# Kernel tuning notes

Hardware: AMD Instinct MI355X
Metric: run time of the kernel (lower is better)

## Reference

```python
import jax, jax.numpy as jnp
import numpy as np

B, N, C = 16, 64, 512


def _ln(x, g, b, eps=1e-5):
    m = x.mean(-1, keepdims=True)
    v = ((x - m) ** 2).mean(-1, keepdims=True)
    return (x - m) * jax.lax.rsqrt(v + eps) * g + b


def _layer(x, edge, WA, WB, WE, WU, WV, ge, be, gv, bv):
    # x: (B, N, C); edge: (B, N, N, C) with edge[b, i, j] for pair (end=i, start=j)
    n = x.shape[1]
    res = x
    Vix = x @ WA.T  # end-node (i) features
    Vjx = x @ WB.T  # start-node (j) features
    e_lin = edge @ WE.T
    # 'ev,bvc->bec' with end/start one-hots == broadcast gather over i / j
    m = Vix[:, :, None, :] + Vjx[:, None, :, :] + e_lin
    edge = edge + jax.nn.relu(_ln(m, ge, be))
    e = jax.nn.softmax(jax.nn.sigmoid(edge), axis=2)  # softmax over start-node axis j
    Ujx = x @ WV.T  # gathered at start node j
    # end.T scatter == sum over j of e[b,i,j,c] * Ujx[b,j,c]
    agg = jnp.einsum('bijc,bjc->bic', e, Ujx) / n
    x = x @ WU.T + agg
    x = jax.nn.relu(res + _ln(x, gv, bv))
    return x, edge


def setup_inputs() -> dict:
    key = jax.random.key(0)
    ks = jax.random.split(key, 12)
    scale = float(np.sqrt(2.0 / C))
    inp = {
        "x": jax.random.normal(ks[0], (B, N, C), jnp.float32),
        "edge": jax.random.normal(ks[1], (B, N * N, C), jnp.float32),
    }
    names = ["WA1", "WB1", "WE1", "WU1", "WV1", "WA2", "WB2", "WE2", "WU2", "WV2"]
    for i, nm in enumerate(names):
        inp[nm] = jax.random.normal(ks[2 + i], (C, C), jnp.float32) * scale
    for nm in ["ge1", "gv1", "ge2", "gv2"]:
        inp[nm] = jnp.ones((C,), jnp.float32)
    for nm in ["be1", "bv1", "be2", "bv2"]:
        inp[nm] = jnp.zeros((C,), jnp.float32)
    return inp


def reference(x, edge, WA1, WB1, WE1, WU1, WV1, WA2, WB2, WE2, WU2, WV2,
              ge1, be1, gv1, bv1, ge2, be2, gv2, bv2):
    b, _, c = edge.shape
    n = x.shape[1]
    edge = edge.reshape(b, n, n, c)
    x, edge = _layer(x, edge, WA1, WB1, WE1, WU1, WV1, ge1, be1, gv1, bv1)
    x, edge = _layer(x, edge, WA2, WB2, WE2, WU2, WV2, ge2, be2, gv2, bv2)
    return x, edge.reshape(b, n * n, c)
```

## Files before the change

kernel.cpp:

```cpp
#include <hip/hip_runtime.h>
#include <math.h>

#define CD 512
#define NNODE 64
#define TPAD 520

typedef __attribute__((ext_vector_type(8)))  short bfrag8;
typedef __attribute__((ext_vector_type(4)))  short sv4;
typedef __attribute__((ext_vector_type(4)))  float f32x4;
typedef __attribute__((ext_vector_type(16))) float f32x16;

__device__ __forceinline__ unsigned short f2bf(float f) {
    union { float f; unsigned u; } v; v.f = f;
    unsigned r = (v.u + 0x7fffu + ((v.u >> 16) & 1u)) >> 16;
    return (unsigned short)r;
}
__device__ __forceinline__ float bf2f(unsigned short u) {
    union { unsigned u; float f; } v; v.u = ((unsigned)u) << 16;
    return v.f;
}

__global__ void pack16_k(const float* __restrict__ W0, const float* __restrict__ W1,
                         const float* __restrict__ W2, const float* __restrict__ W3,
                         const float* __restrict__ W4, const float* __restrict__ W5,
                         const float* __restrict__ W6, const float* __restrict__ W7,
                         unsigned short* __restrict__ out)
{
    const float* Ws[8] = {W0,W1,W2,W3,W4,W5,W6,W7};
    int kt = blockIdx.x, ct = blockIdx.y, wi = blockIdx.z, l = threadIdx.x;
    const float* W = Ws[wi];
    int c  = ct * 16 + (l & 15);
    int k0 = kt * 32 + (l >> 4) * 8;
    const float* src = W + (size_t)c * CD + k0;
    unsigned short o[8];
    #pragma unroll
    for (int i = 0; i < 8; ++i) o[i] = f2bf(src[i]);
    unsigned short* dst = out + (size_t)wi * 262144 + ((size_t)(kt * 32 + ct) * 64 + l) * 8;
    *(bfrag8*)dst = *(bfrag8*)o;
}

__global__ void pack32_k(const float* __restrict__ W0, const float* __restrict__ W1,
                         unsigned short* __restrict__ out)
{
    const float* Ws[2] = {W0,W1};
    int kt = blockIdx.x, ct = blockIdx.y, wi = blockIdx.z, l = threadIdx.x;
    const float* W = Ws[wi];
    int c  = ct * 32 + (l & 31);
    int k0 = kt * 16 + (l >> 5) * 8;
    const float* src = W + (size_t)c * CD + k0;
    unsigned short o[8];
    #pragma unroll
    for (int i = 0; i < 8; ++i) o[i] = f2bf(src[i]);
    unsigned short* dst = out + (size_t)wi * 262144 + ((size_t)(kt * 16 + ct) * 64 + l) * 8;
    *(bfrag8*)dst = *(bfrag8*)o;
}

__global__ __launch_bounds__(256, 2) void gemm4_mfma(
    const float* __restrict__ A, const unsigned short* __restrict__ Bp4,
    float* __restrict__ O0, float* __restrict__ O1,
    float* __restrict__ O2, float* __restrict__ O3)
{
    __shared__ unsigned short atile[16 * TPAD];
    const int rb = blockIdx.x * 16, widx = blockIdx.y;
    float* outs[4] = {O0,O1,O2,O3};
    float* out = outs[widx];
    const unsigned short* Bp = Bp4 + (size_t)widx * 262144;
    const int t = threadIdx.x, l = t & 63, v = t >> 6;

    #pragma unroll
    for (int it = 0; it < 8; ++it) {
        int flat = it * 1024 + t * 4;
        float4 x4 = *(const float4*)(A + (size_t)rb * CD + flat);
        int r = flat >> 9, c = flat & 511;
        sv4 pk; pk.x = (short)f2bf(x4.x); pk.y = (short)f2bf(x4.y);
        pk.z = (short)f2bf(x4.z); pk.w = (short)f2bf(x4.w);
        *(sv4*)(atile + r * TPAD + c) = pk;
    }
    __syncthreads();

    f32x4 acc[8] = {};
    const unsigned short* aptr = atile + (size_t)(l & 15) * TPAD + (l >> 4) * 8;
    const unsigned short* bptr = Bp + (size_t)(v * 8) * 512 + (size_t)l * 8;

    bfrag8 a0, a1, b0[8], b1[8];
    a0 = *(const bfrag8*)aptr;
    #pragma unroll
    for (int tt = 0; tt < 8; ++tt) b0[tt] = *(const bfrag8*)(bptr + tt * 512);
    for (int k2 = 0; k2 < 8; ++k2) {
        int kt1 = 2 * k2 + 1;
        a1 = *(const bfrag8*)(aptr + kt1 * 32);
        #pragma unroll
        for (int tt = 0; tt < 8; ++tt) b1[tt] = *(const bfrag8*)(bptr + (size_t)kt1 * 16384 + tt * 512);
        #pragma unroll
        for (int tt = 0; tt < 8; ++tt)
            acc[tt] = __builtin_amdgcn_mfma_f32_16x16x32_bf16(a0, b0[tt], acc[tt], 0, 0, 0);
        int kt2 = (k2 == 7) ? 15 : (2 * k2 + 2);
        a0 = *(const bfrag8*)(aptr + kt2 * 32);
        #pragma unroll
        for (int tt = 0; tt < 8; ++tt) b0[tt] = *(const bfrag8*)(bptr + (size_t)kt2 * 16384 + tt * 512);
        #pragma unroll
        for (int tt = 0; tt < 8; ++tt)
            acc[tt] = __builtin_amdgcn_mfma_f32_16x16x32_bf16(a1, b1[tt], acc[tt], 0, 0, 0);
    }
    #pragma unroll
    for (int tt = 0; tt < 8; ++tt) {
        int c = (v * 8 + tt) * 16 + (l & 15);
        #pragma unroll
        for (int r = 0; r < 4; ++r) {
            int row = rb + (l >> 4) * 4 + r;
            out[(size_t)row * CD + c] = acc[tt][r];
        }
    }
}

__global__ __launch_bounds__(512, 2) void edge_mfma(
    const float* __restrict__ ein, float* __restrict__ eout,
    const float* __restrict__ Vix, const float* __restrict__ Vjx,
    const float* __restrict__ Ujx, const unsigned short* __restrict__ Bp,
    const float* __restrict__ ge, const float* __restrict__ be,
    float* __restrict__ agg)
{
    __shared__ unsigned short tile[2 * 64 * TPAD];
    __shared__ float sums[128][2][2];

    const int q = blockIdx.x;
    const int b = q >> 5, i0 = q & 31;
    const int bi0 = b * 64 + i0;
    const int t = threadIdx.x, l = t & 63, w = t >> 6;
    const int stripe = w & 3, H = w >> 2, p = stripe >> 1;
    const int brow = b * 64;

    #pragma unroll
    for (int p2 = 0; p2 < 2; ++p2) {
        const float* src = ein + (size_t)(bi0 + p2 * 32) * 32768;
        unsigned short* dst = tile + p2 * 64 * TPAD;
        #pragma unroll 4
        for (int it = 0; it < 16; ++it) {
            int flat = it * 2048 + t * 4;
            float4 v4 = *(const float4*)(src + flat);
            int r = flat >> 9, c = flat & 511;
            sv4 pk; pk.x = (short)f2bf(v4.x); pk.y = (short)f2bf(v4.y);
            pk.z = (short)f2bf(v4.z); pk.w = (short)f2bf(v4.w);
            *(sv4*)(dst + r * TPAD + c) = pk;
        }
    }
    __syncthreads();

    f32x16 acc[8] = {};
    const unsigned short* aptr = tile + (size_t)(stripe * 32 + (l & 31)) * TPAD + (l >> 5) * 8;
    const unsigned short* bptr = Bp + (size_t)(H * 8) * 512 + (size_t)l * 8;

    bfrag8 a0, a1, b0[8], b1[8];
    a0 = *(const bfrag8*)aptr;
    #pragma unroll
    for (int tt = 0; tt < 8; ++tt) b0[tt] = *(const bfrag8*)(bptr + tt * 512);
    for (int k2 = 0; k2 < 16; ++k2) {
        int kt1 = 2 * k2 + 1;
        a1 = *(const bfrag8*)(aptr + kt1 * 16);
        #pragma unroll
        for (int tt = 0; tt < 8; ++tt) b1[tt] = *(const bfrag8*)(bptr + (size_t)kt1 * 8192 + tt * 512);
        #pragma unroll
        for (int tt = 0; tt < 8; ++tt)
            acc[tt] = __builtin_amdgcn_mfma_f32_32x32x16_bf16(a0, b0[tt], acc[tt], 0, 0, 0);
        int kt2 = (k2 == 15) ? 31 : (2 * k2 + 2);
        a0 = *(const bfrag8*)(aptr + kt2 * 16);
        #pragma unroll
        for (int tt = 0; tt < 8; ++tt) b0[tt] = *(const bfrag8*)(bptr + (size_t)kt2 * 8192 + tt * 512);
        #pragma unroll
        for (int tt = 0; tt < 8; ++tt)
            acc[tt] = __builtin_amdgcn_mfma_f32_32x32x16_bf16(a1, b1[tt], acc[tt], 0, 0, 0);
    }

    const int cbase = H * 256 + (l & 31);
    const int biP = bi0 + p * 32;
    float vix[8], gev[8], bev[8];
    #pragma unroll
    for (int tt = 0; tt < 8; ++tt) {
        int c = cbase + tt * 32;
        vix[tt] = Vix[(size_t)biP * CD + c];
        gev[tt] = ge[c]; bev[tt] = be[c];
    }
    float s1[16], s2[16];
    #pragma unroll
    for (int r = 0; r < 16; ++r) {
        int rl = (r & 3) + 8 * (r >> 2) + 4 * (l >> 5);
        int rt = stripe * 32 + rl;
        int j = rt & 63;
        const float* vjr = Vjx + (size_t)(brow + j) * CD;
        float a1_ = 0.f, a2_ = 0.f;
        #pragma unroll
        for (int tt = 0; tt < 8; ++tt) {
            float m = acc[tt][r] + vix[tt] + vjr[cbase + tt * 32];
            acc[tt][r] = m;
            a1_ += m; a2_ = fmaf(m, m, a2_);
        }
        s1[r] = a1_; s2[r] = a2_;
    }
    #pragma unroll
    for (int off = 1; off < 32; off <<= 1) {
        #pragma unroll
        for (int r = 0; r < 16; ++r) {
            s1[r] += __shfl_xor(s1[r], off, 64);
            s2[r] += __shfl_xor(s2[r], off, 64);
        }
    }
    if ((l & 31) == 0) {
        #pragma unroll
        for (int r = 0; r < 16; ++r) {
            int rl = (r & 3) + 8 * (r >> 2) + 4 * (l >> 5);
            int rt = stripe * 32 + rl;
            sums[rt][H][0] = s1[r]; sums[rt][H][1] = s2[r];
        }
    }
    __syncthreads();

    #pragma unroll
    for (int r = 0; r < 16; ++r) {
        int rl = (r & 3) + 8 * (r >> 2) + 4 * (l >> 5);
        int rt = stripe * 32 + rl;
        float t1 = sums[rt][0][0] + sums[rt][1][0];
        float t2 = sums[rt][0][1] + sums[rt][1][1];
        float mean = t1 * (1.f / 512.f);
        float var  = t2 * (1.f / 512.f) - mean * mean;
        float rs   = rsqrtf(var + 1e-5f);
        int j = rt & 63;
        unsigned short* trow = tile + (size_t)rt * TPAD;
        float* erow = eout + ((size_t)biP * 64 + j) * CD;
        #pragma unroll
        for (int tt = 0; tt < 8; ++tt) {
            int c = cbase + tt * 32;
            float ln  = (acc[tt][r] - mean) * rs * gev[tt] + bev[tt];
            float env = bf2f(trow[c]) + fmaxf(ln, 0.f);
            erow[c] = env;
            float sg = 1.f / (1.f + __expf(-env));
            trow[c] = f2bf(__expf(sg));
        }
    }
    __syncthreads();

    {
        int c = t;
        #pragma unroll
        for (int pp = 0; pp < 2; ++pp) {
            const unsigned short* tp = tile + pp * 64 * TPAD;
            const float* uj = Ujx + (size_t)brow * CD + c;
            float den = 0.f, num = 0.f;
            #pragma unroll 8
            for (int j = 0; j < NNODE; ++j) {
                float wv = bf2f(tp[j * TPAD + c]);
                float uv = uj[(size_t)j * CD];
                den += wv; num = fmaf(wv, uv, num);
            }
            agg[(size_t)(bi0 + pp * 32) * CD + c] = num / (den * (float)NNODE);
        }
    }
}

__global__ __launch_bounds__(256) void xupd_kernel(
    const float* __restrict__ res,
    const float* __restrict__ XU,
    const float* __restrict__ aggp,
    const float* __restrict__ gv, const float* __restrict__ bv,
    float* __restrict__ xout)
{
    int r = blockIdx.x * 4 + (threadIdx.x >> 6);
    int lane = threadIdx.x & 63;
    const float* xu = XU + (size_t)r * CD;
    const float* ag = aggp + (size_t)r * CD;
    float y[8]; float s1 = 0.f, s2 = 0.f;
    #pragma unroll
    for (int u = 0; u < 8; ++u) {
        int c = lane + u * 64;
        float v = xu[c] + ag[c];
        y[u] = v; s1 += v; s2 += v * v;
    }
    #pragma unroll
    for (int off = 32; off > 0; off >>= 1) {
        s1 += __shfl_xor(s1, off, 64);
        s2 += __shfl_xor(s2, off, 64);
    }
    float mean = s1 * (1.f / 512.f);
    float var  = s2 * (1.f / 512.f) - mean * mean;
    float rs   = rsqrtf(var + 1e-5f);
    const float* rr = res + (size_t)r * CD;
    float* xo = xout + (size_t)r * CD;
    #pragma unroll
    for (int u = 0; u < 8; ++u) {
        int c = lane + u * 64;
        float ln = (y[u] - mean) * rs * gv[c] + bv[c];
        xo[c] = fmaxf(rr[c] + ln, 0.f);
    }
}

extern "C" void kernel_launch(void* const* d_in, const int* in_sizes, int n_in,
                              void* d_out, int out_size, void* d_ws, size_t ws_size,
                              hipStream_t stream)
{
    const float* x    = (const float*)d_in[0];
    const float* edge = (const float*)d_in[1];
    const float* W[10];
    for (int i = 0; i < 10; ++i) W[i] = (const float*)d_in[2 + i];
    const float* ge1 = (const float*)d_in[12];
    const float* gv1 = (const float*)d_in[13];
    const float* ge2 = (const float*)d_in[14];
    const float* gv2 = (const float*)d_in[15];
    const float* be1 = (const float*)d_in[16];
    const float* bv1 = (const float*)d_in[17];
    const float* be2 = (const float*)d_in[18];
    const float* bv2 = (const float*)d_in[19];

    char* wsb = (char*)d_ws;
    unsigned short* P16 = (unsigned short*)wsb;
    unsigned short* P32 = (unsigned short*)(wsb + (size_t)4  * 1048576);
    float* Vix = (float*)(wsb + (size_t)5  * 1048576);
    float* Vjx = (float*)(wsb + (size_t)7  * 1048576);
    float* Ujx = (float*)(wsb + (size_t)9  * 1048576);
    float* XU  = (float*)(wsb + (size_t)11 * 1048576);
    float* agg = (float*)(wsb + (size_t)13 * 1048576);
    float* x1  = (float*)(wsb + (size_t)15 * 1048576);

    float* xout = (float*)d_out;
    float* eint = xout + (size_t)524288;

    pack16_k<<<dim3(16, 32, 8), 64, 0, stream>>>(
        W[0], W[1], W[4], W[3], W[5], W[6], W[9], W[8], P16);
    pack32_k<<<dim3(32, 16, 2), 64, 0, stream>>>(W[2], W[7], P32);

    gemm4_mfma<<<dim3(64, 4), 256, 0, stream>>>(x, P16, Vix, Vjx, Ujx, XU);
    edge_mfma<<<512, 512, 0, stream>>>(edge, eint, Vix, Vjx, Ujx, P32, ge1, be1, agg);
    xupd_kernel<<<256, 256, 0, stream>>>(x, XU, agg, gv1, bv1, x1);
    gemm4_mfma<<<dim3(64, 4), 256, 0, stream>>>(x1, P16 + (size_t)4 * 262144, Vix, Vjx, Ujx, XU);
    edge_mfma<<<512, 512, 0, stream>>>(eint, eint, Vix, Vjx, Ujx, P32 + 262144, ge2, be2, agg);
    xupd_kernel<<<256, 256, 0, stream>>>(x1, XU, agg, gv2, bv2, xout);
}
```

Before: 591.7 us.

## Store intermediate edge tensor in bf16 and retile edge/projection kernels per node row

The layer-1 edge output is now written as bf16 into the output buffer and read back as bf16 by layer 2, which is meant to cut memory traffic on the largest tensor. The edge kernel now handles one end-node row per block (1024 blocks, occupancy hint raised to 4) with fewer accumulators per wave, and the node projection GEMM switches to 32x32 MFMA tiles over 64-row blocks. All weight packing goes through a single pack kernel. The trade-off is extra rounding in the residual edge carried between layers, which costs some accuracy.

```diff
diff --git a/kernel.cpp b/kernel.cpp
--- a/kernel.cpp
+++ b/kernel.cpp
@@ -6,8 +6,8 @@
 #define TPAD 520
 
 typedef __attribute__((ext_vector_type(8)))  short bfrag8;
+typedef __attribute__((ext_vector_type(8)))  short sv8;
 typedef __attribute__((ext_vector_type(4)))  short sv4;
-typedef __attribute__((ext_vector_type(4)))  float f32x4;
 typedef __attribute__((ext_vector_type(16))) float f32x16;
 
 __device__ __forceinline__ unsigned short f2bf(float f) {
@@ -20,29 +20,14 @@
     return v.f;
 }
 
-__global__ void pack16_k(const float* __restrict__ W0, const float* __restrict__ W1,
+__global__ void pack32_k(const float* __restrict__ W0, const float* __restrict__ W1,
                          const float* __restrict__ W2, const float* __restrict__ W3,
                          const float* __restrict__ W4, const float* __restrict__ W5,
                          const float* __restrict__ W6, const float* __restrict__ W7,
+                         const float* __restrict__ W8, const float* __restrict__ W9,
                          unsigned short* __restrict__ out)
 {
-    const float* Ws[8] = {W0,W1,W2,W3,W4,W5,W6,W7};
-    int kt = blockIdx.x, ct = blockIdx.y, wi = blockIdx.z, l = threadIdx.x;
-    const float* W = Ws[wi];
-    int c  = ct * 16 + (l & 15);
-    int k0 = kt * 32 + (l >> 4) * 8;
-    const float* src = W + (size_t)c * CD + k0;
-    unsigned short o[8];
-    #pragma unroll
-    for (int i = 0; i < 8; ++i) o[i] = f2bf(src[i]);
-    unsigned short* dst = out + (size_t)wi * 262144 + ((size_t)(kt * 32 + ct) * 64 + l) * 8;
-    *(bfrag8*)dst = *(bfrag8*)o;
-}
-
-__global__ void pack32_k(const float* __restrict__ W0, const float* __restrict__ W1,
-                         unsigned short* __restrict__ out)
-{
-    const float* Ws[2] = {W0,W1};
+    const float* Ws[10] = {W0,W1,W2,W3,W4,W5,W6,W7,W8,W9};
     int kt = blockIdx.x, ct = blockIdx.y, wi = blockIdx.z, l = threadIdx.x;
     const float* W = Ws[wi];
     int c  = ct * 32 + (l & 31);
@@ -55,85 +40,92 @@
     *(bfrag8*)dst = *(bfrag8*)o;
 }
 
-__global__ __launch_bounds__(256, 2) void gemm4_mfma(
+__global__ __launch_bounds__(512, 4) void proj_mfma(
     const float* __restrict__ A, const unsigned short* __restrict__ Bp4,
     float* __restrict__ O0, float* __restrict__ O1,
     float* __restrict__ O2, float* __restrict__ O3)
 {
-    __shared__ unsigned short atile[16 * TPAD];
-    const int rb = blockIdx.x * 16, widx = blockIdx.y;
+    __shared__ unsigned short tile[64 * TPAD];
+    const int rb = blockIdx.x * 64, widx = blockIdx.y;
     float* outs[4] = {O0,O1,O2,O3};
     float* out = outs[widx];
     const unsigned short* Bp = Bp4 + (size_t)widx * 262144;
-    const int t = threadIdx.x, l = t & 63, v = t >> 6;
-
-    #pragma unroll
-    for (int it = 0; it < 8; ++it) {
-        int flat = it * 1024 + t * 4;
-        float4 x4 = *(const float4*)(A + (size_t)rb * CD + flat);
+    const int t = threadIdx.x, l = t & 63, w = t >> 6;
+    const int stripe = w & 1, H = w >> 1;
+
+    const float* src = A + (size_t)rb * CD;
+    #pragma unroll 4
+    for (int it = 0; it < 16; ++it) {
+        int flat = it * 2048 + t * 4;
+        float4 v4 = *(const float4*)(src + flat);
         int r = flat >> 9, c = flat & 511;
-        sv4 pk; pk.x = (short)f2bf(x4.x); pk.y = (short)f2bf(x4.y);
-        pk.z = (short)f2bf(x4.z); pk.w = (short)f2bf(x4.w);
-        *(sv4*)(atile + r * TPAD + c) = pk;
+        sv4 pk; pk.x = (short)f2bf(v4.x); pk.y = (short)f2bf(v4.y);
+        pk.z = (short)f2bf(v4.z); pk.w = (short)f2bf(v4.w);
+        *(sv4*)(tile + r * TPAD + c) = pk;
     }
     __syncthreads();
 
-    f32x4 acc[8] = {};
-    const unsigned short* aptr = atile + (size_t)(l & 15) * TPAD + (l >> 4) * 8;
-    const unsigned short* bptr = Bp + (size_t)(v * 8) * 512 + (size_t)l * 8;
-
-    bfrag8 a0, a1, b0[8], b1[8];
+    f32x16 acc[4] = {};
+    const unsigned short* aptr = tile + (size_t)(stripe * 32 + (l & 31)) * TPAD + (l >> 5) * 8;
+    const unsigned short* bptr = Bp + ((size_t)(H * 4) * 64 + l) * 8;
+
+    bfrag8 a0, a1, b0[4], b1[4];
     a0 = *(const bfrag8*)aptr;
     #pragma unroll
-    for (int tt = 0; tt < 8; ++tt) b0[tt] = *(const bfrag8*)(bptr + tt * 512);
-    for (int k2 = 0; k2 < 8; ++k2) {
+    for (int tt = 0; tt < 4; ++tt) b0[tt] = *(const bfrag8*)(bptr + tt * 512);
+    for (int k2 = 0; k2 < 16; ++k2) {
         int kt1 = 2 * k2 + 1;
-        a1 = *(const bfrag8*)(aptr + kt1 * 32);
-        #pragma unroll
-        for (int tt = 0; tt < 8; ++tt) b1[tt] = *(const bfrag8*)(bptr + (size_t)kt1 * 16384 + tt * 512);
-        #pragma unroll
-        for (int tt = 0; tt < 8; ++tt)
-            acc[tt] = __builtin_amdgcn_mfma_f32_16x16x32_bf16(a0, b0[tt], acc[tt], 0, 0, 0);
-        int kt2 = (k2 == 7) ? 15 : (2 * k2 + 2);
-        a0 = *(const bfrag8*)(aptr + kt2 * 32);
-        #pragma unroll
-        for (int tt = 0; tt < 8; ++tt) b0[tt] = *(const bfrag8*)(bptr + (size_t)kt2 * 16384 + tt * 512);
-        #pragma unroll
-        for (int tt = 0; tt < 8; ++tt)
-            acc[tt] = __builtin_amdgcn_mfma_f32_16x16x32_bf16(a1, b1[tt], acc[tt], 0, 0, 0);
-    }
-    #pragma unroll
-    for (int tt = 0; tt < 8; ++tt) {
-        int c = (v * 8 + tt) * 16 + (l & 15);
-        #pragma unroll
-        for (int r = 0; r < 4; ++r) {
-            int row = rb + (l >> 4) * 4 + r;
-            out[(size_t)row * CD + c] = acc[tt][r];
-        }
-    }
-}
-
-__global__ __launch_bounds__(512, 2) void edge_mfma(
-    const float* __restrict__ ein, float* __restrict__ eout,
+        a1 = *(const bfrag8*)(aptr + kt1 * 16);
+        #pragma unroll
+        for (int tt = 0; tt < 4; ++tt) b1[tt] = *(const bfrag8*)(bptr + (size_t)kt1 * 8192 + tt * 512);
+        #pragma unroll
+        for (int tt = 0; tt < 4; ++tt)
+            acc[tt] = __builtin_amdgcn_mfma_f32_32x32x16_bf16(a0, b0[tt], acc[tt], 0, 0, 0);
+        int kt2 = (k2 == 15) ? 31 : (2 * k2 + 2);
+        a0 = *(const bfrag8*)(aptr + kt2 * 16);
+        #pragma unroll
+        for (int tt = 0; tt < 4; ++tt) b0[tt] = *(const bfrag8*)(bptr + (size_t)kt2 * 8192 + tt * 512);
+        #pragma unroll
+        for (int tt = 0; tt < 4; ++tt)
+            acc[tt] = __builtin_amdgcn_mfma_f32_32x32x16_bf16(a1, b1[tt], acc[tt], 0, 0, 0);
+    }
+    const int cbase = H * 128 + (l & 31);
+    #pragma unroll
+    for (int r = 0; r < 16; ++r) {
+        int rl = (r & 3) + 8 * (r >> 2) + 4 * (l >> 5);
+        int row = rb + stripe * 32 + rl;
+        #pragma unroll
+        for (int tt = 0; tt < 4; ++tt)
+            out[(size_t)row * CD + cbase + tt * 32] = acc[tt][r];
+    }
+}
+
+template<bool INBF, bool OUTBF>
+__global__ __launch_bounds__(512, 4) void edge_mfma(
+    const void* __restrict__ einv, void* __restrict__ eoutv,
     const float* __restrict__ Vix, const float* __restrict__ Vjx,
     const float* __restrict__ Ujx, const unsigned short* __restrict__ Bp,
     const float* __restrict__ ge, const float* __restrict__ be,
     float* __restrict__ agg)
 {
-    __shared__ unsigned short tile[2 * 64 * TPAD];
-    __shared__ float sums[128][2][2];
-
-    const int q = blockIdx.x;
-    const int b = q >> 5, i0 = q & 31;
-    const int bi0 = b * 64 + i0;
+    __shared__ unsigned short tile[64 * TPAD];
+    __shared__ float sums[64][4][2];
+
+    const int bi = blockIdx.x;
+    const int brow = bi & ~63;
     const int t = threadIdx.x, l = t & 63, w = t >> 6;
-    const int stripe = w & 3, H = w >> 2, p = stripe >> 1;
-    const int brow = b * 64;
-
-    #pragma unroll
-    for (int p2 = 0; p2 < 2; ++p2) {
-        const float* src = ein + (size_t)(bi0 + p2 * 32) * 32768;
-        unsigned short* dst = tile + p2 * 64 * TPAD;
+    const int stripe = w & 1, H = w >> 1;
+
+    if (INBF) {
+        const unsigned short* src = (const unsigned short*)einv + (size_t)bi * 65536;
+        #pragma unroll 4
+        for (int it = 0; it < 8; ++it) {
+            int flat = it * 4096 + t * 8;
+            int r = flat >> 9, c = flat & 511;
+            *(sv8*)(tile + r * TPAD + c) = *(const sv8*)(src + flat);
+        }
+    } else {
+        const float* src = (const float*)einv + (size_t)bi * 32768;
         #pragma unroll 4
         for (int it = 0; it < 16; ++it) {
             int flat = it * 2048 + t * 4;
@@ -141,43 +133,42 @@
             int r = flat >> 9, c = flat & 511;
             sv4 pk; pk.x = (short)f2bf(v4.x); pk.y = (short)f2bf(v4.y);
             pk.z = (short)f2bf(v4.z); pk.w = (short)f2bf(v4.w);
-            *(sv4*)(dst + r * TPAD + c) = pk;
+            *(sv4*)(tile + r * TPAD + c) = pk;
         }
     }
     __syncthreads();
 
-    f32x16 acc[8] = {};
+    f32x16 acc[4] = {};
     const unsigned short* aptr = tile + (size_t)(stripe * 32 + (l & 31)) * TPAD + (l >> 5) * 8;
-    const unsigned short* bptr = Bp + (size_t)(H * 8) * 512 + (size_t)l * 8;
-
-    bfrag8 a0, a1, b0[8], b1[8];
+    const unsigned short* bptr = Bp + ((size_t)(H * 4) * 64 + l) * 8;
+
+    bfrag8 a0, a1, b0[4], b1[4];
     a0 = *(const bfrag8*)aptr;
     #pragma unroll
-    for (int tt = 0; tt < 8; ++tt) b0[tt] = *(const bfrag8*)(bptr + tt * 512);
+    for (int tt = 0; tt < 4; ++tt) b0[tt] = *(const bfrag8*)(bptr + tt * 512);
     for (int k2 = 0; k2 < 16; ++k2) {
         int kt1 = 2 * k2 + 1;
         a1 = *(const bfrag8*)(aptr + kt1 * 16);
         #pragma unroll
-        for (int tt = 0; tt < 8; ++tt) b1[tt] = *(const bfrag8*)(bptr + (size_t)kt1 * 8192 + tt * 512);
-        #pragma unroll
-        for (int tt = 0; tt < 8; ++tt)
+        for (int tt = 0; tt < 4; ++tt) b1[tt] = *(const bfrag8*)(bptr + (size_t)kt1 * 8192 + tt * 512);
+        #pragma unroll
+        for (int tt = 0; tt < 4; ++tt)
             acc[tt] = __builtin_amdgcn_mfma_f32_32x32x16_bf16(a0, b0[tt], acc[tt], 0, 0, 0);
         int kt2 = (k2 == 15) ? 31 : (2 * k2 + 2);
         a0 = *(const bfrag8*)(aptr + kt2 * 16);
         #pragma unroll
-        for (int tt = 0; tt < 8; ++tt) b0[tt] = *(const bfrag8*)(bptr + (size_t)kt2 * 8192 + tt * 512);
-        #pragma unroll
-        for (int tt = 0; tt < 8; ++tt)
+        for (int tt = 0; tt < 4; ++tt) b0[tt] = *(const bfrag8*)(bptr + (size_t)kt2 * 8192 + tt * 512);
+        #pragma unroll
+        for (int tt = 0; tt < 4; ++tt)
             acc[tt] = __builtin_amdgcn_mfma_f32_32x32x16_bf16(a1, b1[tt], acc[tt], 0, 0, 0);
     }
 
-    const int cbase = H * 256 + (l & 31);
-    const int biP = bi0 + p * 32;
-    float vix[8], gev[8], bev[8];
-    #pragma unroll
-    for (int tt = 0; tt < 8; ++tt) {
+    const int cbase = H * 128 + (l & 31);
+    float vix[4], gev[4], bev[4];
+    #pragma unroll
+    for (int tt = 0; tt < 4; ++tt) {
         int c = cbase + tt * 32;
-        vix[tt] = Vix[(size_t)biP * CD + c];
+        vix[tt] = Vix[(size_t)bi * CD + c];
         gev[tt] = ge[c]; bev[tt] = be[c];
     }
     float s1[16], s2[16];
@@ -185,11 +176,10 @@
     for (int r = 0; r < 16; ++r) {
         int rl = (r & 3) + 8 * (r >> 2) + 4 * (l >> 5);
         int rt = stripe * 32 + rl;
-        int j = rt & 63;
-        const float* vjr = Vjx + (size_t)(brow + j) * CD;
+        const float* vjr = Vjx + (size_t)(brow + rt) * CD;
         float a1_ = 0.f, a2_ = 0.f;
         #pragma unroll
-        for (int tt = 0; tt < 8; ++tt) {
+        for (int tt = 0; tt < 4; ++tt) {
             float m = acc[tt][r] + vix[tt] + vjr[cbase + tt * 32];
             acc[tt][r] = m;
             a1_ += m; a2_ = fmaf(m, m, a2_);
@@ -218,20 +208,19 @@
     for (int r = 0; r < 16; ++r) {
         int rl = (r & 3) + 8 * (r >> 2) + 4 * (l >> 5);
         int rt = stripe * 32 + rl;
-        float t1 = sums[rt][0][0] + sums[rt][1][0];
-        float t2 = sums[rt][0][1] + sums[rt][1][1];
+        float t1 = sums[rt][0][0] + sums[rt][1][0] + sums[rt][2][0] + sums[rt][3][0];
+        float t2 = sums[rt][0][1] + sums[rt][1][1] + sums[rt][2][1] + sums[rt][3][1];
         float mean = t1 * (1.f / 512.f);
         float var  = t2 * (1.f / 512.f) - mean * mean;
         float rs   = rsqrtf(var + 1e-5f);
-        int j = rt & 63;
         unsigned short* trow = tile + (size_t)rt * TPAD;
-        float* erow = eout + ((size_t)biP * 64 + j) * CD;
-        #pragma unroll
-        for (int tt = 0; tt < 8; ++tt) {
+        #pragma unroll
+        for (int tt = 0; tt < 4; ++tt) {
             int c = cbase + tt * 32;
             float ln  = (acc[tt][r] - mean) * rs * gev[tt] + bev[tt];
             float env = bf2f(trow[c]) + fmaxf(ln, 0.f);
-            erow[c] = env;
+            if (OUTBF) ((unsigned short*)eoutv)[(size_t)bi * 65536 + rt * 512 + c] = f2bf(env);
+            else       ((float*)eoutv)[(size_t)bi * 32768 + rt * 512 + c] = env;
             float sg = 1.f / (1.f + __expf(-env));
             trow[c] = f2bf(__expf(sg));
         }
@@ -240,19 +229,15 @@
 
     {
         int c = t;
-        #pragma unroll
-        for (int pp = 0; pp < 2; ++pp) {
-            const unsigned short* tp = tile + pp * 64 * TPAD;
-            const float* uj = Ujx + (size_t)brow * CD + c;
-            float den = 0.f, num = 0.f;
-            #pragma unroll 8
-            for (int j = 0; j < NNODE; ++j) {
-                float wv = bf2f(tp[j * TPAD + c]);
-                float uv = uj[(size_t)j * CD];
-                den += wv; num = fmaf(wv, uv, num);
-            }
-            agg[(size_t)(bi0 + pp * 32) * CD + c] = num / (den * (float)NNODE);
-        }
+        const float* uj = Ujx + (size_t)brow * CD + c;
+        float den = 0.f, num = 0.f;
+        #pragma unroll 8
+        for (int j = 0; j < NNODE; ++j) {
+            float wv = bf2f(tile[j * TPAD + c]);
+            float uv = uj[(size_t)j * CD];
+            den += wv; num = fmaf(wv, uv, num);
+        }
+        agg[(size_t)bi * CD + c] = num / (den * (float)NNODE);
     }
 }
 
@@ -310,26 +295,28 @@
     const float* bv2 = (const float*)d_in[19];
 
     char* wsb = (char*)d_ws;
-    unsigned short* P16 = (unsigned short*)wsb;
-    unsigned short* P32 = (unsigned short*)(wsb + (size_t)4  * 1048576);
-    float* Vix = (float*)(wsb + (size_t)5  * 1048576);
-    float* Vjx = (float*)(wsb + (size_t)7  * 1048576);
-    float* Ujx = (float*)(wsb + (size_t)9  * 1048576);
-    float* XU  = (float*)(wsb + (size_t)11 * 1048576);
-    float* agg = (float*)(wsb + (size_t)13 * 1048576);
-    float* x1  = (float*)(wsb + (size_t)15 * 1048576);
-
-    float* xout = (float*)d_out;
-    float* eint = xout + (size_t)524288;
-
-    pack16_k<<<dim3(16, 32, 8), 64, 0, stream>>>(
-        W[0], W[1], W[4], W[3], W[5], W[6], W[9], W[8], P16);
-    pack32_k<<<dim3(32, 16, 2), 64, 0, stream>>>(W[2], W[7], P32);
-
-    gemm4_mfma<<<dim3(64, 4), 256, 0, stream>>>(x, P16, Vix, Vjx, Ujx, XU);
-    edge_mfma<<<512, 512, 0, stream>>>(edge, eint, Vix, Vjx, Ujx, P32, ge1, be1, agg);
+    unsigned short* P32 = (unsigned short*)wsb;
+    float* Vix = (float*)(wsb + (size_t)6  * 1048576);
+    float* Vjx = (float*)(wsb + (size_t)8  * 1048576);
+    float* Ujx = (float*)(wsb + (size_t)10 * 1048576);
+    float* XU  = (float*)(wsb + (size_t)12 * 1048576);
+    float* agg = (float*)(wsb + (size_t)14 * 1048576);
+    float* x1  = (float*)(wsb + (size_t)16 * 1048576);
+
+    float* xout  = (float*)d_out;
+    float* eintF = xout + (size_t)524288;
+
+    pack32_k<<<dim3(32, 16, 10), 64, 0, stream>>>(
+        W[0], W[1], W[4], W[3], W[5], W[6], W[9], W[8], W[2], W[7], P32);
+
+#define PW(i) (P32 + (size_t)(i) * 262144)
+    proj_mfma<<<dim3(16, 4), 512, 0, stream>>>(x, PW(0), Vix, Vjx, Ujx, XU);
+    edge_mfma<false, true><<<1024, 512, 0, stream>>>(edge, eintF, Vix, Vjx, Ujx,
+                                                     PW(8), ge1, be1, agg);
     xupd_kernel<<<256, 256, 0, stream>>>(x, XU, agg, gv1, bv1, x1);
-    gemm4_mfma<<<dim3(64, 4), 256, 0, stream>>>(x1, P16 + (size_t)4 * 262144, Vix, Vjx, Ujx, XU);
-    edge_mfma<<<512, 512, 0, stream>>>(eint, eint, Vix, Vjx, Ujx, P32 + 262144, ge2, be2, agg);
+    proj_mfma<<<dim3(16, 4), 512, 0, stream>>>(x1, PW(4), Vix, Vjx, Ujx, XU);
+    edge_mfma<true, false><<<1024, 512, 0, stream>>>(eintF, eintF, Vix, Vjx, Ujx,
+                                                     PW(9), ge2, be2, agg);
     xupd_kernel<<<256, 256, 0, stream>>>(x1, XU, agg, gv2, bv2, xout);
-}
+#undef PW
+}
```

Measured after the change: 498.7 us. 1.19x faster.
